# Kernel tuning notes

Measured on AMD Instinct MI355X. Metric: run time of the kernel, lower is better.

## Reference

```python
import jax, jax.numpy as jnp
import numpy as np

B, N, DIN, DOUT = 8, 2048, 256, 256

def setup_inputs() -> dict:
    key = jax.random.key(0)
    k1, k2, k3 = jax.random.split(key, 3)
    H = jax.random.normal(k1, (B, N, DIN), dtype=jnp.float32)
    G = jax.random.uniform(k2, (B, N, N), dtype=jnp.float32)  # positive -> nonzero row/col sums
    # xavier_uniform-style scale for the weight
    limit = float(np.sqrt(6.0 / (DIN + DOUT)))
    W = jax.random.uniform(k3, (DIN, DOUT), dtype=jnp.float32, minval=-limit, maxval=limit)
    return {"H": H, "G": G, "W": W}

def reference(H, G, W):
    # N_e = H @ W : [b,n,dout]
    N_e = H @ W
    # symmetric part
    G_F = (G + jnp.swapaxes(G, 1, 2)) * 0.5
    # loop over k of outer products == two normalized Gram matrices:
    # G_Sin[i,j] = sum_k G[k,i]*G[k,j] / rowsum_k  == G^T diag(1/rowsum) G
    # G_So[i,j]  = sum_k G[i,k]*G[j,k] / colsum_k  == G diag(1/colsum) G^T
    rs = G.sum(axis=-1)  # [b,n] row sums
    cs = G.sum(axis=-2)  # [b,n] col sums
    G_Sin = jnp.einsum('bki,bkj->bij', G / rs[:, :, None], G)
    G_So = jnp.einsum('bik,bjk->bij', G / cs[:, None, :], G)
    H_out = jnp.concatenate([
        jax.nn.relu(G_F @ N_e),
        jax.nn.relu(G_Sin @ N_e),
        jax.nn.relu(G_So @ N_e),
    ], axis=-1)  # [b,n,3*dout]
    return H_out
```

## Files before the change

### kernel.cpp

```cpp
#include <hip/hip_runtime.h>
#include <hip/hip_bf16.h>


constexpr int NN = 2048;
constexpr long GSTR = (long)NN * NN;
constexpr long SDN = 256L * 2048;

using frag8   = __attribute__((ext_vector_type(8))) short;
using floatx4 = __attribute__((ext_vector_type(4))) float;
using ush8    = __attribute__((ext_vector_type(8))) unsigned short;

__device__ inline unsigned short f2bf(float x) {
    unsigned u = __float_as_uint(x);
    u += 0x7FFF + ((u >> 16) & 1);
    return (unsigned short)(u >> 16);
}
__device__ inline float bf2f(unsigned short h) {
    return __uint_as_float((unsigned)h << 16);
}
__device__ inline ushort2 pk2(float a, float b) {
    union { __hip_bfloat162 h; ushort2 u; } cv;
    cv.h = __float22bfloat162_rn(float2{a, b});
    return cv.u;
}
__device__ inline void gload_lds16(const void* g, void* l) {
    __builtin_amdgcn_global_load_lds(
        (const __attribute__((address_space(1))) void*)g,
        (__attribute__((address_space(3))) void*)l, 16, 0, 0);
}

template <int PHASE>
__global__ __launch_bounds__(256) void gemmF(
    const unsigned short* __restrict__ Aa,
    const unsigned short* __restrict__ Ab,
    const unsigned short* __restrict__ Gb,
    const unsigned short* __restrict__ GbT,
    unsigned short* __restrict__ C0,
    unsigned short* __restrict__ C1,
    float* __restrict__ outp,
    const float* __restrict__ s0,
    const float* __restrict__ s1)
{
    constexpr int TM = 256, NT = 32;
    __shared__ __align__(16) unsigned short SH[2][(TM + 64) * 64];

    const int bx = blockIdx.x;
    const int bb = bx & 7;
    const int rr_ = bx >> 3;
    const int jt = rr_ & 31;
    const int h  = rr_ >> 5;
    const int j0 = jt * 64;

    const unsigned short* Ap =
        ((PHASE == 1 && h) ? Ab : Aa) + (long)bb * SDN;
    const unsigned short* Bp =
        (((PHASE == 0) == (h == 0)) ? Gb : GbT) + (long)bb * GSTR;

    const int t = threadIdx.x;
    const int w = t >> 6, l = t & 63;
    const int wm = w >> 1, wn = w & 1;
    const int quad = l >> 4, c15 = l & 15;
    const int lr = l >> 3, ls = l & 7;

    floatx4 acc[8][2] = {};

    auto stage = [&](int buf, int k0) {
        const unsigned short* Bt = Bp + (((long)(j0 >> 7) * 16 + (k0 >> 7)) << 14);
        const int rb = j0 & 127, kin = k0 & 127;
        #pragma unroll
        for (int q = 0; q < 2; ++q) {
            const int rt = q * 32 + w * 8;
            gload_lds16(Bt + (rb + rt + lr) * 128 + kin + ((ls ^ lr) << 3),
                        &SH[buf][TM * 64 + rt * 64]);
        }
        #pragma unroll
        for (int q = 0; q < 8; ++q) {
            const int rt = q * 32 + w * 8;
            gload_lds16(Ap + (long)(rt + lr) * 2048 + k0 + ((ls ^ lr) << 3),
                        &SH[buf][rt * 64]);
        }
    };

    stage(0, 0);
    asm volatile("s_waitcnt vmcnt(0)" ::: "memory");
    __builtin_amdgcn_s_barrier();
    __builtin_amdgcn_sched_barrier(0);

    int cur = 0;
    for (int tt = 0; tt < NT; ++tt) {
        if (tt + 1 < NT) stage(cur ^ 1, (tt + 1) << 6);
        __builtin_amdgcn_sched_barrier(0);
        #pragma unroll
        for (int ks = 0; ks < 2; ++ks) {
            frag8 af[8], bfv[2];
            const int swr = c15 & 7;
            #pragma unroll
            for (int mt = 0; mt < 8; ++mt)
                af[mt] = *(const frag8*)&SH[cur][(wm * 128 + mt * 16 + c15) * 64
                                                + (((ks * 4 + quad) ^ swr) << 3)];
            #pragma unroll
            for (int nt = 0; nt < 2; ++nt)
                bfv[nt] = *(const frag8*)&SH[cur][TM * 64 + (wn * 32 + nt * 16 + c15) * 64
                                                 + (((ks * 4 + quad) ^ swr) << 3)];
            #pragma unroll
            for (int mt = 0; mt < 8; ++mt)
                #pragma unroll
                for (int nt = 0; nt < 2; ++nt)
                    acc[mt][nt] = __builtin_amdgcn_mfma_f32_16x16x32_bf16(
                        af[mt], bfv[nt], acc[mt][nt], 0, 0, 0);
        }
        if (tt + 1 < NT) {
            asm volatile("s_waitcnt vmcnt(0)" ::: "memory");
            __builtin_amdgcn_s_barrier();
            __builtin_amdgcn_sched_barrier(0);
        }
        cur ^= 1;
    }

    __syncthreads();

    if constexpr (PHASE == 0) {
        unsigned short* T16 = &SH[0][0];
        #pragma unroll
        for (int nt = 0; nt < 2; ++nt) {
            const int jc = wn * 32 + nt * 16 + c15;
            const float sc = (h ? s1 : s0)[(long)bb * 2048 + j0 + jc];
            #pragma unroll
            for (int mt = 0; mt < 8; ++mt) {
                const floatx4 v = acc[mt][nt];
                const int ib = wm * 128 + mt * 16 + quad * 4;
                #pragma unroll
                for (int e = 0; e < 4; ++e)
                    T16[(ib + e) * 72 + jc] = f2bf(v[e] * sc);
            }
        }
        __syncthreads();
        unsigned short* Co = (h ? C1 : C0) + ((long)bb * 256 + t) * 2048 + j0;
        const unsigned short* Tr = T16 + t * 72;
        #pragma unroll
        for (int c2 = 0; c2 < 8; ++c2)
            *(ush8*)(Co + c2 * 8) = *(const ush8*)(Tr + c2 * 8);
    } else {
        float* TF = (float*)&SH[0][0];
        #pragma unroll
        for (int nt = 0; nt < 2; ++nt) {
            const int jc = wn * 32 + nt * 16 + c15;
            #pragma unroll
            for (int mt = 0; mt < 8; ++mt) {
                const floatx4 v = acc[mt][nt];
                const int ib = wm * 128 + mt * 16 + quad * 4;
                #pragma unroll
                for (int e = 0; e < 4; ++e)
                    TF[jc * 260 + ib + e] = fmaxf(v[e], 0.f);
            }
        }
        __syncthreads();
        const int jr = t >> 2, iq = t & 3;
        float* Op = outp + ((long)bb * 2048 + j0 + jr) * 768 + (h ? 512 : 256) + iq * 64;
        const float* Sp = TF + jr * 260 + iq * 64;
        #pragma unroll
        for (int c2 = 0; c2 < 16; ++c2)
            *(float4*)(Op + c2 * 4) = *(const float4*)(Sp + c2 * 4);

        if (h == 0) {
            const int w0 = t >> 6, l0 = t & 63;
            const int rg0 = l0 >> 3, c0 = l0 & 7;
            const int ib0 = w0 * 64 + rg0 * 8;
            const int jb0 = j0 + c0 * 8;
            const long ab = (long)bb * SDN;

            union RowU { ush8 v; unsigned u4[4]; unsigned short a[8]; };
            RowU r1[8], r2[8], c1[8], c2v[8];
            #pragma unroll
            for (int r = 0; r < 8; ++r) {
                r1[r].v = *(const ush8*)(Aa + ab + (long)(ib0 + r) * 2048 + jb0);
                r2[r].v = *(const ush8*)(Ab + ab + (long)(ib0 + r) * 2048 + jb0);
            }
            #pragma unroll
            for (int p = 0; p < 4; ++p)
                #pragma unroll
                for (int k = 0; k < 4; ++k) {
                    const unsigned a1 = r1[2*p].u4[k], b1 = r1[2*p+1].u4[k];
                    c1[2*k].u4[p]   = (a1 & 0xffffu) | (b1 << 16);
                    c1[2*k+1].u4[p] = (a1 >> 16) | (b1 & 0xffff0000u);
                    const unsigned a2 = r2[2*p].u4[k], b2 = r2[2*p+1].u4[k];
                    c2v[2*k].u4[p]   = (a2 & 0xffffu) | (b2 << 16);
                    c2v[2*k+1].u4[p] = (a2 >> 16) | (b2 & 0xffff0000u);
                }
            #pragma unroll
            for (int jj = 0; jj < 8; ++jj) {
                const int j = jb0 + jj;
                const float rr = s0[(long)bb * 2048 + j];
                const float cc = s1[(long)bb * 2048 + j];
                float4 o0, o1;
                o0.x = fmaxf(0.5f * (bf2f(c1[jj].a[0]) * rr + bf2f(c2v[jj].a[0]) * cc), 0.f);
                o0.y = fmaxf(0.5f * (bf2f(c1[jj].a[1]) * rr + bf2f(c2v[jj].a[1]) * cc), 0.f);
                o0.z = fmaxf(0.5f * (bf2f(c1[jj].a[2]) * rr + bf2f(c2v[jj].a[2]) * cc), 0.f);
                o0.w = fmaxf(0.5f * (bf2f(c1[jj].a[3]) * rr + bf2f(c2v[jj].a[3]) * cc), 0.f);
                o1.x = fmaxf(0.5f * (bf2f(c1[jj].a[4]) * rr + bf2f(c2v[jj].a[4]) * cc), 0.f);
                o1.y = fmaxf(0.5f * (bf2f(c1[jj].a[5]) * rr + bf2f(c2v[jj].a[5]) * cc), 0.f);
                o1.z = fmaxf(0.5f * (bf2f(c1[jj].a[6]) * rr + bf2f(c2v[jj].a[6]) * cc), 0.f);
                o1.w = fmaxf(0.5f * (bf2f(c1[jj].a[7]) * rr + bf2f(c2v[jj].a[7]) * cc), 0.f);
                float* op = outp + ((long)bb * 2048 + j) * 768 + ib0;
                *(float4*)op       = o0;
                *(float4*)(op + 4) = o1;
            }
        }
    }
}

__global__ __launch_bounds__(256) void gemmNE(
    const float* __restrict__ H,
    const unsigned short* __restrict__ Wt,
    unsigned short* __restrict__ NeT)
{
    constexpr int TM = 64, K = 256;
    __shared__ __align__(16) unsigned short As[TM * 64];
    __shared__ __align__(16) unsigned short Bs[64 * 64];

    const int t  = threadIdx.x;
    const int bx = blockIdx.x;
    const int xcd = bx & 7;
    const int kk  = bx >> 3;
    const int itile = xcd + 8 * (kk >> 5);
    const int rem   = kk & 31;
    const int bb    = rem >> 2;
    const int jt    = rem & 3;
    const int i0b = itile * TM;
    const int j0  = jt * 64;

    const unsigned short* Btb = Wt + (long)j0 * K;
    const float* Af = H + (long)bb * (2048L * 256);

    const int w = t >> 6, l = t & 63;
    const int wm = w >> 1, wn = w & 1;
    const int quad = l >> 4, c15 = l & 15;
    const int lr = l >> 3, ls = l & 7;

    floatx4 acc[2][2] = {};

    for (int k0 = 0; k0 < K; k0 += 64) {
        const int ar  = t >> 2;
        const int ac0 = (t & 3) * 2;
        const float* ap = Af + (long)(i0b + ar) * 256 + k0 + ac0 * 8;
        const float4 x0 = *(const float4*)(ap + 0);
        const float4 x1 = *(const float4*)(ap + 4);
        const float4 x2 = *(const float4*)(ap + 8);
        const float4 x3 = *(const float4*)(ap + 12);
        union { ush8 v; ushort2 u2[4]; } p0, p1;
        p0.u2[0] = pk2(x0.x, x0.y); p0.u2[1] = pk2(x0.z, x0.w);
        p0.u2[2] = pk2(x1.x, x1.y); p0.u2[3] = pk2(x1.z, x1.w);
        p1.u2[0] = pk2(x2.x, x2.y); p1.u2[1] = pk2(x2.z, x2.w);
        p1.u2[2] = pk2(x3.x, x3.y); p1.u2[3] = pk2(x3.z, x3.w);
        const int sw = ar & 7;
        *(ush8*)&As[ar * 64 + ((ac0 ^ sw) << 3)]       = p0.v;
        *(ush8*)&As[ar * 64 + (((ac0 + 1) ^ sw) << 3)] = p1.v;
        #pragma unroll
        for (int q = 0; q < 2; ++q) {
            const int rt = w * 16 + q * 8;
            gload_lds16(Btb + (long)(rt + lr) * K + k0 + ((ls ^ lr) << 3),
                        &Bs[rt * 64]);
        }
        __syncthreads();

        #pragma unroll
        for (int ks = 0; ks < 2; ++ks) {
            frag8 af[2], bfv[2];
            const int swr = c15 & 7;
            #pragma unroll
            for (int mt = 0; mt < 2; ++mt)
                af[mt] = *(const frag8*)&As[(wm * 32 + mt * 16 + c15) * 64
                                            + (((ks * 4 + quad) ^ swr) << 3)];
            #pragma unroll
            for (int nt = 0; nt < 2; ++nt)
                bfv[nt] = *(const frag8*)&Bs[(wn * 32 + nt * 16 + c15) * 64
                                             + (((ks * 4 + quad) ^ swr) << 3)];
            #pragma unroll
            for (int mt = 0; mt < 2; ++mt)
                #pragma unroll
                for (int nt = 0; nt < 2; ++nt)
                    acc[mt][nt] = __builtin_amdgcn_mfma_f32_16x16x32_bf16(
                        af[mt], bfv[nt], acc[mt][nt], 0, 0, 0);
        }
        __syncthreads();
    }

    #pragma unroll
    for (int mt = 0; mt < 2; ++mt) {
        const int ib = i0b + wm * 32 + mt * 16 + quad * 4;
        #pragma unroll
        for (int nt = 0; nt < 2; ++nt) {
            const floatx4 v = acc[mt][nt];
            const int gj = j0 + wn * 32 + nt * 16 + c15;
            union { ushort4 v; ushort2 u2[2]; } p;
            p.u2[0] = pk2(v[0], v[1]); p.u2[1] = pk2(v[2], v[3]);
            *(ushort4*)(NeT + ((long)bb * 256 + gj) * 2048 + ib) = p.v;
        }
    }
}

__global__ __launch_bounds__(256) void cvt_stream(
    const float* __restrict__ G,
    unsigned short* __restrict__ Gbf,
    float* __restrict__ pcs,
    float* __restrict__ inv_rs, float* __restrict__ rs_raw)
{
    __shared__ float sm[4][16];
    const int b  = blockIdx.y;
    const int s  = blockIdx.x;
    const int i0 = s * 16;
    const int t  = threadIdx.x;
    const int c8 = t * 8;
    const int w  = t >> 6, l = t & 63;

    const float* gp = G + (long)b * GSTR + (long)i0 * NN + c8;
    unsigned short* gb = Gbf + (long)b * GSTR;
    const int tc = c8 >> 7, cin = c8 & 127;

    float csum[8] = {};
    float rp[16];

    #pragma unroll
    for (int r = 0; r < 16; ++r) {
        const float4 x0 = *(const float4*)(gp + (long)r * NN);
        const float4 x1 = *(const float4*)(gp + (long)r * NN + 4);
        union { ush8 v; ushort2 u2[4]; } pk;
        pk.u2[0] = pk2(x0.x, x0.y); pk.u2[1] = pk2(x0.z, x0.w);
        pk.u2[2] = pk2(x1.x, x1.y); pk.u2[3] = pk2(x1.z, x1.w);
        const int gi = i0 + r;
        *(ush8*)(gb + (((long)(gi >> 7) * 16 + tc) << 14) + ((gi & 127) << 7) + cin) = pk.v;
        rp[r] = x0.x + x0.y + x0.z + x0.w + x1.x + x1.y + x1.z + x1.w;
        csum[0] += x0.x; csum[1] += x0.y; csum[2] += x0.z; csum[3] += x0.w;
        csum[4] += x1.x; csum[5] += x1.y; csum[6] += x1.z; csum[7] += x1.w;
    }

    float* pp = pcs + ((long)b * 128 + s) * NN + c8;
    *(float4*)pp       = make_float4(csum[0], csum[1], csum[2], csum[3]);
    *(float4*)(pp + 4) = make_float4(csum[4], csum[5], csum[6], csum[7]);

    #pragma unroll
    for (int r = 0; r < 16; ++r) {
        rp[r] += __shfl_xor(rp[r], 1);
        rp[r] += __shfl_xor(rp[r], 2);
        rp[r] += __shfl_xor(rp[r], 4);
        rp[r] += __shfl_xor(rp[r], 8);
        rp[r] += __shfl_xor(rp[r], 16);
        rp[r] += __shfl_xor(rp[r], 32);
    }
    if (l == 0) {
        #pragma unroll
        for (int r = 0; r < 16; ++r) sm[w][r] = rp[r];
    }
    __syncthreads();
    if (t < 16) {
        const float s_ = sm[0][t] + sm[1][t] + sm[2][t] + sm[3][t];
        rs_raw[(long)b * NN + i0 + t] = s_;
        inv_rs[(long)b * NN + i0 + t] = 1.0f / s_;
    }
}

__global__ __launch_bounds__(256) void cvt_t(
    const unsigned short* __restrict__ Gbf, unsigned short* __restrict__ GbfT)
{
    const int b  = blockIdx.z;
    const int tr = blockIdx.y, tc = blockIdx.x;
    const long src = (long)b * GSTR + (((long)tr * 16 + tc) << 14);
    const long dst = (long)b * GSTR + (((long)tc * 16 + tr) << 14);
    const int t = threadIdx.x;
    const int w = t >> 6, l = t & 63;
    const int wm = w >> 1, wn = w & 1;
    const int rg = l >> 3, c = l & 7;
    const int il = wm * 64 + rg * 8;
    const int jl = wn * 64 + c * 8;

    union RowU { ush8 v; unsigned u4[4]; };
    RowU rows[8], cols[8];
    #pragma unroll
    for (int r = 0; r < 8; ++r)
        rows[r].v = *(const ush8*)(Gbf + src + (long)(il + r) * 128 + jl);
    __builtin_amdgcn_sched_barrier(0);

    #pragma unroll
    for (int p = 0; p < 4; ++p)
        #pragma unroll
        for (int k = 0; k < 4; ++k) {
            const unsigned a = rows[2 * p].u4[k], bq = rows[2 * p + 1].u4[k];
            cols[2 * k].u4[p]     = (a & 0xffffu) | (bq << 16);
            cols[2 * k + 1].u4[p] = (a >> 16) | (bq & 0xffff0000u);
        }
    #pragma unroll
    for (int j = 0; j < 8; ++j)
        *(ush8*)(GbfT + dst + (long)(jl + j) * 128 + il) = cols[j].v;
}

__global__ __launch_bounds__(256) void finalize(
    const float* __restrict__ pcs,
    float* __restrict__ inv_cs, float* __restrict__ cs_raw,
    const float* __restrict__ W, unsigned short* __restrict__ Wt)
{
    const int idx = blockIdx.x * 256 + threadIdx.x;
    if (blockIdx.y == 0) {
        const int b = idx >> 11, i = idx & 2047;
        float s = 0.f;
        for (int ic = 0; ic < 128; ++ic) s += pcs[((long)b * 128 + ic) * NN + i];
        inv_cs[idx] = 1.0f / s;
        cs_raw[idx] = s;
    } else {
        #pragma unroll
        for (int e = 0; e < 4; ++e) {
            const int flat = idx * 4 + e;
            const int j = flat >> 8, k = flat & 255;
            Wt[flat] = f2bf(W[(long)k * 256 + j]);
        }
    }
}

extern "C" void kernel_launch(void* const* d_in, const int* in_sizes, int n_in,
                              void* d_out, int out_size, void* d_ws, size_t ws_size,
                              hipStream_t stream)
{
    constexpr int B = 8;
    const float* H = (const float*)d_in[0];
    const float* G = (const float*)d_in[1];
    const float* W = (const float*)d_in[2];
    float* out = (float*)d_out;

    unsigned short* ws16 = (unsigned short*)d_ws;
    unsigned short* Gbf  = ws16;
    unsigned short* GbfT = Gbf  + (long)B * GSTR;
    unsigned short* Wt   = GbfT + (long)B * GSTR;
    unsigned short* NeT  = Wt   + 65536;
    unsigned short* M1sT = NeT  + 4194304;
    unsigned short* M2sT = M1sT + 4194304;
    float* inv_rs = (float*)(M2sT + 4194304);
    float* rs_raw = inv_rs + 16384;
    float* inv_cs = rs_raw + 16384;
    float* cs_raw = inv_cs + 16384;
    float* pcs    = cs_raw + 16384;

    cvt_stream<<<dim3(128, 8), 256, 0, stream>>>(G, Gbf, pcs, inv_rs, rs_raw);
    cvt_t<<<dim3(16, 16, 8), 256, 0, stream>>>(Gbf, GbfT);
    finalize<<<dim3(64, 2), 256, 0, stream>>>(pcs, inv_cs, cs_raw, W, Wt);

    gemmNE<<<1024, 256, 0, stream>>>(H, Wt, NeT);
    gemmF<0><<<512, 256, 0, stream>>>(NeT, nullptr, Gbf, GbfT,
                                      M1sT, M2sT, nullptr, inv_rs, inv_cs);
    gemmF<1><<<512, 256, 0, stream>>>(M1sT, M2sT, Gbf, GbfT,
                                      nullptr, nullptr, out, rs_raw, cs_raw);
}
```

Baseline: 359.2 us.

## Switch GEMM main loop to 4-stage BK=32 pipeline with partial vmcnt waits

The GEMM k-loop moves from double-buffered 64-wide k tiles to a four-buffer ring of 32-wide k tiles, keeping three tiles of loads in flight. It waits with partial vmcnt counts instead of draining all loads each iteration. The LDS swizzle is redone for the 32-element row width. This aims to hide global-to-LDS latency better, at the cost of twice as many barriers and smaller compute chunks per sync.

Result: slower. 372.9 us (+3.8%).

```diff
diff --git a/kernel.cpp b/kernel.cpp
--- a/kernel.cpp
+++ b/kernel.cpp
@@ -41,8 +41,10 @@
     const float* __restrict__ s0,
     const float* __restrict__ s1)
 {
-    constexpr int TM = 256, NT = 32;
-    __shared__ __align__(16) unsigned short SH[2][(TM + 64) * 64];
+    constexpr int TM = 256, BK = 32, NT = 64;
+    constexpr int ASZ = TM * BK;
+    constexpr int BSZ = 64 * BK;
+    __shared__ __align__(16) unsigned short SH[4][ASZ + BSZ];
 
     const int bx = blockIdx.x;
     const int bb = bx & 7;
@@ -60,62 +62,72 @@
     const int w = t >> 6, l = t & 63;
     const int wm = w >> 1, wn = w & 1;
     const int quad = l >> 4, c15 = l & 15;
-    const int lr = l >> 3, ls = l & 7;
+    const int lr = l >> 2, ls = l & 3;
+    const int g  = (ls - (lr >> 1)) & 3;
 
     floatx4 acc[8][2] = {};
 
-    auto stage = [&](int buf, int k0) {
+    auto stage = [&](int buf, int tt) {
+        const int k0 = tt << 5;
         const unsigned short* Bt = Bp + (((long)(j0 >> 7) * 16 + (k0 >> 7)) << 14);
         const int rb = j0 & 127, kin = k0 & 127;
-        #pragma unroll
-        for (int q = 0; q < 2; ++q) {
-            const int rt = q * 32 + w * 8;
-            gload_lds16(Bt + (rb + rt + lr) * 128 + kin + ((ls ^ lr) << 3),
-                        &SH[buf][TM * 64 + rt * 64]);
-        }
-        #pragma unroll
-        for (int q = 0; q < 8; ++q) {
-            const int rt = q * 32 + w * 8;
-            gload_lds16(Ap + (long)(rt + lr) * 2048 + k0 + ((ls ^ lr) << 3),
-                        &SH[buf][rt * 64]);
+        {
+            const int rt = w * 16;
+            gload_lds16(Bt + (rb + rt + lr) * 128 + kin + (g << 3),
+                        &SH[buf][ASZ + rt * BK]);
+        }
+        #pragma unroll
+        for (int q = 0; q < 4; ++q) {
+            const int rt = q * 64 + w * 16;
+            gload_lds16(Ap + (long)(rt + lr) * 2048 + k0 + (g << 3),
+                        &SH[buf][rt * BK]);
         }
     };
 
-    stage(0, 0);
+    auto compute = [&](int cur) {
+        frag8 af[8], bfv[2];
+        #pragma unroll
+        for (int mt = 0; mt < 8; ++mt) {
+            const int row = wm * 128 + mt * 16 + c15;
+            af[mt] = *(const frag8*)&SH[cur][row * BK
+                                             + (((quad + (row >> 1)) & 3) << 3)];
+        }
+        #pragma unroll
+        for (int nt = 0; nt < 2; ++nt) {
+            const int row = wn * 32 + nt * 16 + c15;
+            bfv[nt] = *(const frag8*)&SH[cur][ASZ + row * BK
+                                              + (((quad + (row >> 1)) & 3) << 3)];
+        }
+        #pragma unroll
+        for (int mt = 0; mt < 8; ++mt)
+            #pragma unroll
+            for (int nt = 0; nt < 2; ++nt)
+                acc[mt][nt] = __builtin_amdgcn_mfma_f32_16x16x32_bf16(
+                    af[mt], bfv[nt], acc[mt][nt], 0, 0, 0);
+    };
+
+    stage(0, 0); stage(1, 1); stage(2, 2);
+
+    for (int tt = 0; tt < NT - 3; ++tt) {
+        asm volatile("s_waitcnt vmcnt(10)" ::: "memory");
+        __builtin_amdgcn_s_barrier();
+        __builtin_amdgcn_sched_barrier(0);
+        stage((tt + 3) & 3, tt + 3);
+        __builtin_amdgcn_sched_barrier(0);
+        compute(tt & 3);
+    }
+    asm volatile("s_waitcnt vmcnt(10)" ::: "memory");
+    __builtin_amdgcn_s_barrier();
+    __builtin_amdgcn_sched_barrier(0);
+    compute((NT - 3) & 3);
+    asm volatile("s_waitcnt vmcnt(5)" ::: "memory");
+    __builtin_amdgcn_s_barrier();
+    __builtin_amdgcn_sched_barrier(0);
+    compute((NT - 2) & 3);
     asm volatile("s_waitcnt vmcnt(0)" ::: "memory");
     __builtin_amdgcn_s_barrier();
     __builtin_amdgcn_sched_barrier(0);
-
-    int cur = 0;
-    for (int tt = 0; tt < NT; ++tt) {
-        if (tt + 1 < NT) stage(cur ^ 1, (tt + 1) << 6);
-        __builtin_amdgcn_sched_barrier(0);
-        #pragma unroll
-        for (int ks = 0; ks < 2; ++ks) {
-            frag8 af[8], bfv[2];
-            const int swr = c15 & 7;
-            #pragma unroll
-            for (int mt = 0; mt < 8; ++mt)
-                af[mt] = *(const frag8*)&SH[cur][(wm * 128 + mt * 16 + c15) * 64
-                                                + (((ks * 4 + quad) ^ swr) << 3)];
-            #pragma unroll
-            for (int nt = 0; nt < 2; ++nt)
-                bfv[nt] = *(const frag8*)&SH[cur][TM * 64 + (wn * 32 + nt * 16 + c15) * 64
-                                                 + (((ks * 4 + quad) ^ swr) << 3)];
-            #pragma unroll
-            for (int mt = 0; mt < 8; ++mt)
-                #pragma unroll
-                for (int nt = 0; nt < 2; ++nt)
-                    acc[mt][nt] = __builtin_amdgcn_mfma_f32_16x16x32_bf16(
-                        af[mt], bfv[nt], acc[mt][nt], 0, 0, 0);
-        }
-        if (tt + 1 < NT) {
-            asm volatile("s_waitcnt vmcnt(0)" ::: "memory");
-            __builtin_amdgcn_s_barrier();
-            __builtin_amdgcn_sched_barrier(0);
-        }
-        cur ^= 1;
-    }
+    compute((NT - 1) & 3);
 
     __syncthreads();
 
```
